# Optimization experiments

Measured on AMD Instinct MI355X. Metric: run time of the kernel, lower is better.

The kernel has to match this reference:

```python
import jax, jax.numpy as jnp
import numpy as np

B, T, D, DFF = 8, 2048, 1024, 4096
EPS = 1e-6
PLIF_ALPHA = 2.0


@jax.custom_vjp
def spike_fn(m):
    # hard threshold forward, atan surrogate backward (PLIF neuron)
    return (m > 0.0).astype(m.dtype)

def _spk_fwd(m):
    return (m > 0.0).astype(m.dtype), m

def _spk_bwd(m, g):
    ds = PLIF_ALPHA / (2.0 * (1.0 + (jnp.pi * 0.5 * PLIF_ALPHA * m) ** 2))
    return (g * ds,)

spike_fn.defvjp(_spk_fwd, _spk_bwd)


def _rmsnorm(x, w):
    rstd = jax.lax.rsqrt(jnp.mean(x * x, axis=-1, keepdims=True) + EPS)
    return x * rstd * w


def setup_inputs() -> dict:
    key = jax.random.key(0)
    ks = jax.random.split(key, 9)
    sc = 0.02
    return {
        'x': jax.random.normal(ks[0], (B, T, D), jnp.float32),
        'rms_w1': jnp.ones((D,), jnp.float32),
        'rms_w2': jnp.ones((D,), jnp.float32),
        'delta_w': sc * jax.random.normal(ks[1], (D, D), jnp.float32),
        'delta_b': jnp.zeros((D,), jnp.float32),
        'b_w': sc * jax.random.normal(ks[2], (D, D), jnp.float32),
        'b_b': jnp.zeros((D,), jnp.float32),
        'A_log': jnp.log(jnp.linspace(0.5, 2.0, D).astype(jnp.float32)),
        'log_tau': jnp.full((D,), jnp.log(2.0), jnp.float32),
        'plif_thr': jnp.ones((D,), jnp.float32),
        'syn_w': sc * jax.random.normal(ks[3], (D, D), jnp.float32),
        'syn_b': jnp.zeros((D,), jnp.float32),
        'gate_w': sc * jax.random.normal(ks[4], (D, D), jnp.float32),
        'gate_b': jnp.zeros((D,), jnp.float32),
        'ffn_g_w': sc * jax.random.normal(ks[5], (DFF, D), jnp.float32),
        'ffn_u_w': sc * jax.random.normal(ks[6], (DFF, D), jnp.float32),
        'ffn_d_w': sc * jax.random.normal(ks[7], (D, DFF), jnp.float32),
    }


def _forward(x, rms_w1, rms_w2, delta_w, delta_b, b_w, b_b, A_log, log_tau,
             plif_thr, syn_w, syn_b, gate_w, gate_b, ffn_g_w, ffn_u_w, ffn_d_w):
    Bx, Tx, Dx = x.shape
    # --- RMSNorm 1 ---
    y1 = _rmsnorm(x, rms_w1)
    # --- selective-scan style liquid inputs ---
    delta = jax.nn.softplus(jnp.einsum('btd,ed->bte', y1, delta_w) + delta_b)  # [B,T,D]
    bvec = delta * (jnp.einsum('btd,ed->bte', y1, b_w) + b_b)                  # [B,T,D]
    A = jnp.exp(-delta * jnp.exp(A_log))                                        # [B,T,D]

    # --- liquid recurrent scan: h_t = tanh(A_t * h_{t-1} + b_t) ---
    def liquid_step(h, ab):
        a_t, b_t = ab
        h = jnp.tanh(a_t * h + b_t)
        return h, h

    h0 = jnp.zeros((Bx, Dx), x.dtype)
    _, h_post = jax.lax.scan(liquid_step, h0,
                             (jnp.swapaxes(A, 0, 1), jnp.swapaxes(bvec, 0, 1)))
    h_post = jnp.swapaxes(h_post, 0, 1)  # [B,T,D]

    # --- PLIF spiking scan with soft reset ---
    pdec = jnp.exp(-1.0 / jnp.exp(log_tau))  # [D]

    def plif_step(v, h_t):
        v_pre = pdec * v + (1.0 - pdec) * h_t
        s = spike_fn(v_pre - plif_thr)
        return v_pre - s * plif_thr, s

    v0 = jnp.zeros((Bx, Dx), x.dtype)
    _, spike = jax.lax.scan(plif_step, v0, jnp.swapaxes(h_post, 0, 1))
    spike = jnp.swapaxes(spike, 0, 1)

    # --- SEW shortcut + synaptic gate ---
    spike_in = spike + h_post
    syn = jnp.einsum('btd,ed->bte', spike_in, syn_w) + syn_b
    gate = jax.nn.sigmoid(jnp.einsum('btd,ed->bte', spike_in, gate_w) + gate_b)
    x1 = x + syn * gate

    # --- RMSNorm 2 + SwiGLU FFN + residual ---
    y2 = _rmsnorm(x1, rms_w2)
    ffn_act = jax.nn.silu(y2 @ ffn_g_w.T) * (y2 @ ffn_u_w.T)
    return x1 + ffn_act @ ffn_d_w.T


def reference(x, rms_w1, rms_w2, delta_w, delta_b, b_w, b_b, A_log, log_tau,
              plif_thr, syn_w, syn_b, gate_w, gate_b, ffn_g_w, ffn_u_w, ffn_d_w):
    return _forward(x, rms_w1, rms_w2, delta_w, delta_b, b_w, b_b, A_log,
                    log_tau, plif_thr, syn_w, syn_b, gate_w, gate_b,
                    ffn_g_w, ffn_u_w, ffn_d_w)
```

## Files before the change

kernel.cpp:

```cpp
#include <hip/hip_runtime.h>
#include <stdint.h>

#define B_   8
#define T_   2048
#define D_   1024
#define DFF_ 4096
#define M_   (B_ * T_)

typedef __bf16 bf16;
typedef bf16  bf16x8 __attribute__((ext_vector_type(8)));
typedef bf16  bf16x4 __attribute__((ext_vector_type(4)));
typedef float f32x4  __attribute__((ext_vector_type(4)));

#define CAST_LDS(p) ((__attribute__((address_space(3))) void*)(p))
#define CAST_GLB(p) ((const __attribute__((address_space(1))) void*)(p))

struct CatArgs {
    const float* w1[3];
    const float* w2[3];
    bf16* dst[3];
    int end[3];
};

__global__ __launch_bounds__(256) void cvt_cat16_kernel(CatArgs a) {
    const int b = blockIdx.x;
    const int seg = (b >= a.end[0] ? 1 : 0) + (b >= a.end[1] ? 1 : 0);
    const int d = b - (seg ? a.end[seg - 1] : 0);
    const int rr = d & 31;
    const float* src = ((rr < 16) ? a.w1[seg] : a.w2[seg]) +
                       (size_t)(((d >> 5) << 4) + (d & 15)) * D_;
    bf16* dst = a.dst[seg] + (size_t)d * D_;
    const int t = threadIdx.x;
    const float4 v = ((const float4*)src)[t];
    bf16x4 o;
    o[0] = (bf16)v.x; o[1] = (bf16)v.y; o[2] = (bf16)v.z; o[3] = (bf16)v.w;
    ((bf16x4*)dst)[t] = o;
}

__global__ __launch_bounds__(256) void cvt_plain_kernel(const float* __restrict__ s,
                                                        bf16* __restrict__ d) {
    const int i = (blockIdx.x * 256 + threadIdx.x) * 4;
    const float4 v = *(const float4*)(s + i);
    bf16x4 o;
    o[0] = (bf16)v.x; o[1] = (bf16)v.y; o[2] = (bf16)v.z; o[3] = (bf16)v.w;
    *(bf16x4*)(d + i) = o;
}

__global__ __launch_bounds__(256) void rmsnorm_kernel(const float* __restrict__ x,
                                                      const float* __restrict__ w,
                                                      bf16* __restrict__ y) {
    const size_t row = blockIdx.x;
    const int t = threadIdx.x;
    const float4 v = ((const float4*)(x + row * D_))[t];
    float ss = v.x * v.x + v.y * v.y + v.z * v.z + v.w * v.w;
#pragma unroll
    for (int off = 32; off; off >>= 1) ss += __shfl_down(ss, off);
    __shared__ float red[4];
    if ((t & 63) == 0) red[t >> 6] = ss;
    __syncthreads();
    const float total = red[0] + red[1] + red[2] + red[3];
    const float rstd = rsqrtf(total * (1.0f / (float)D_) + 1e-6f);
    const float4 wv = ((const float4*)w)[t];
    bf16x4 o;
    o[0] = (bf16)(v.x * rstd * wv.x);
    o[1] = (bf16)(v.y * rstd * wv.y);
    o[2] = (bf16)(v.z * rstd * wv.z);
    o[3] = (bf16)(v.w * rstd * wv.w);
    ((bf16x4*)(y + row * D_))[t] = o;
}

__global__ __launch_bounds__(256) void rmsnorm_bf_kernel(const bf16* __restrict__ x,
                                                         const float* __restrict__ w,
                                                         bf16* __restrict__ y) {
    const size_t row = blockIdx.x;
    const int t = threadIdx.x;
    const bf16x4 xv = ((const bf16x4*)(x + row * D_))[t];
    float f0 = (float)xv[0], f1 = (float)xv[1], f2 = (float)xv[2], f3 = (float)xv[3];
    float ss = f0 * f0 + f1 * f1 + f2 * f2 + f3 * f3;
#pragma unroll
    for (int off = 32; off; off >>= 1) ss += __shfl_down(ss, off);
    __shared__ float red[4];
    if ((t & 63) == 0) red[t >> 6] = ss;
    __syncthreads();
    const float total = red[0] + red[1] + red[2] + red[3];
    const float rstd = rsqrtf(total * (1.0f / (float)D_) + 1e-6f);
    const float4 wv = ((const float4*)w)[t];
    bf16x4 o;
    o[0] = (bf16)(f0 * rstd * wv.x);
    o[1] = (bf16)(f1 * rstd * wv.y);
    o[2] = (bf16)(f2 * rstd * wv.z);
    o[3] = (bf16)(f3 * rstd * wv.w);
    ((bf16x4*)(y + row * D_))[t] = o;
}

#define SCAN_C  32
#define SCAN_L  (T_ / SCAN_C)
#define SCAN_W  32
#define SCAN_PF 8

template <int N, int W0>
__device__ __forceinline__ void scan_body(const uint32_t* __restrict__ p,
                                          bf16* __restrict__ o, const int ts,
                                          const float pdec, const float om,
                                          const float th) {
    uint32_t buf[SCAN_PF];
#pragma unroll
    for (int i = 0; i < SCAN_PF; ++i) buf[i] = p[(size_t)i * D_];
    float h = 0.0f, v = 0.0f;
#pragma unroll 8
    for (int k = 0; k < N; ++k) {
        const uint32_t w = buf[k & (SCAN_PF - 1)];
        if (k + SCAN_PF < N) buf[k & (SCAN_PF - 1)] = p[(size_t)(k + SCAN_PF) * D_];
        const float a  = __builtin_bit_cast(float, w << 16);
        const float bb = __builtin_bit_cast(float, w & 0xffff0000u);
        const float xv = fmaf(a, h, bb);
        const float e2 = __expf(2.0f * xv);
        h = 1.0f - __fdividef(2.0f, 1.0f + e2);
        const float vpre = fmaf(pdec, v, om * h);
        const float s = (vpre > th) ? 1.0f : 0.0f;
        v = vpre - s * th;
        if (k >= W0) o[(size_t)(ts + k) * D_] = (bf16)(s + h);
    }
}

__global__ __launch_bounds__(256) void scan_kernel(const uint32_t* __restrict__ ABp,
                                                   const float* __restrict__ log_tau,
                                                   const float* __restrict__ thr,
                                                   bf16* __restrict__ sp) {
    const int g = blockIdx.x * 256 + threadIdx.x;
    const int d = g & (D_ - 1);
    const int bc = g >> 10;
    const int b = bc / SCAN_C;
    const int c = bc % SCAN_C;
    const float pdec = __expf(-__expf(-log_tau[d]));
    const float om = 1.0f - pdec;
    const float th = thr[d];
    const int t0 = c * SCAN_L;
    const uint32_t* base = ABp + (size_t)b * (T_ * D_) + d;
    bf16* o = sp + (size_t)b * (T_ * D_) + d;
    if (c == 0) {
        scan_body<SCAN_L, 0>(base, o, 0, pdec, om, th);
    } else {
        const int ts = t0 - SCAN_W;
        scan_body<SCAN_L + SCAN_W, SCAN_W>(base + (size_t)ts * D_, o, ts, pdec, om, th);
    }
}


#define STG_A(kt, par, kh)                                                             \
  { bf16* l_ = lA0 + (((par) << 1) + (kh)) * 8192;                                     \
    const bf16* g_ = gA + (kt) * 64 + ((kh) << 5);                                     \
    __builtin_amdgcn_global_load_lds(CAST_GLB(g_), CAST_LDS(l_), 16, 0, 0);            \
    __builtin_amdgcn_global_load_lds(CAST_GLB(g_ + g2), CAST_LDS(l_ + 4096), 16, 0, 0); }
#define STG_B(gb, kt, par, kh)                                                         \
  { bf16* l_ = lB0 + (((par) << 1) + (kh)) * 8192;                                     \
    const bf16* g_ = (gb) + (kt) * 64 + ((kh) << 5);                                   \
    __builtin_amdgcn_global_load_lds(CAST_GLB(g_), CAST_LDS(l_), 16, 0, 0);            \
    __builtin_amdgcn_global_load_lds(CAST_GLB(g_ + g2), CAST_LDS(l_ + 4096), 16, 0, 0); }
#define DSREAD_A(KS, MH)                                                               \
  { const bf16* As_ = smA + (cb + (KS)) * 8192 + swz;                                  \
    _Pragma("unroll")                                                                  \
    for (int i = 0; i < 4; ++i)                                                        \
      af[i] = *(const bf16x8*)(As_ + (mr128 + (MH) * 64 + i * 16 + lane15) * 32);      \
  }
#define DSREAD_B(KS)                                                                   \
  { const bf16* Bs_ = smB + (cb + (KS)) * 8192 + swz;                                  \
    _Pragma("unroll")                                                                  \
    for (int j = 0; j < 4; ++j)                                                        \
      bfr[j] = *(const bf16x8*)(Bs_ + (nc64 + j * 16 + lane15) * 32);                  \
  }
#define MFMA16(MH)                                                                     \
  __builtin_amdgcn_s_setprio(1);                                                       \
  _Pragma("unroll")                                                                    \
  for (int i = 0; i < 4; ++i)                                                          \
    _Pragma("unroll")                                                                  \
    for (int j = 0; j < 4; ++j)                                                        \
      acc[(MH) * 4 + i][j] = __builtin_amdgcn_mfma_f32_16x16x32_bf16(                  \
          af[i], bfr[j], acc[(MH) * 4 + i][j], 0, 0, 0);                               \
  __builtin_amdgcn_s_setprio(0);
#define GBAR() __builtin_amdgcn_s_barrier()
#define LGKM0() asm volatile("s_waitcnt lgkmcnt(0)" ::: "memory")

template <int MODE>
__global__ __launch_bounds__(512, 2) void gemm8p_kernel(
    const bf16* __restrict__ A, const bf16* __restrict__ Bw,
    const int K, const int Nlog, const int NTN,
    const float* __restrict__ b1, const float* __restrict__ b2,
    const float* __restrict__ extra, const bf16* __restrict__ extra_bf,
    void* __restrict__ outp) {
    __shared__ bf16 smem[65536] __attribute__((aligned(16)));
    bf16* const smA = smem;
    bf16* const smB = smem + 32768;

    const int tid = threadIdx.x;
    const int wave = tid >> 6;
    const int lane = tid & 63;
    const int lane15 = lane & 15;
    const int quad = lane >> 4;
    const int mr = wave >> 2;
    const int nc = wave & 3;
    const int mr128 = mr * 128;
    const int nc64 = nc * 64;
    const int swz = (quad ^ ((lane15 >> 1) & 3)) << 3;

    const int xcd = blockIdx.x & 7;
    const int cu  = blockIdx.x >> 3;
    const int mt  = xcd * 8 + (cu & 7);
    const int nt0 = cu >> 3;
    const int TPB = NTN >> 2;
    const int NT  = K >> 6;
    const int S   = TPB * NT;

    const int srow = tid >> 2;
    const int scol = (((tid & 3) ^ ((srow >> 1) & 3)) << 3);
    const bf16* const gA = A + (size_t)(mt * 256 + srow) * K + scol;
    const size_t g2 = (size_t)128 * K;
    const size_t dB = (size_t)1024 * K;
    const bf16* gBc = Bw + (size_t)(nt0 * 256 + srow) * K + scol;
    bf16* const lA0 = smA + (wave << 9);
    bf16* const lB0 = smB + (wave << 9);

    f32x4 acc[8][4] = {};
    bf16x8 af[4];
    bf16x8 bfr[4];

    STG_B(gBc, 0, 0, 0); STG_A(0, 0, 0); STG_B(gBc, 0, 0, 1); STG_A(0, 0, 1);
    asm volatile("s_waitcnt vmcnt(4)" ::: "memory");
    STG_B(gBc, 1, 1, 0); STG_A(1, 1, 0); STG_B(gBc, 1, 1, 1);
    asm volatile("s_waitcnt vmcnt(6)" ::: "memory");
    GBAR();

    for (int w = 0; w < TPB; ++w) {
        const bf16* const gBn = gBc + dB;
        for (int t = 0; t < NT; ++t) {
            const int s = w * NT + t;
            const int cb = (t & 1) << 1;
            const int tp1 = (t + 1 == NT) ? 0 : t + 1;
            const int tp2 = (t + 2 >= NT) ? t + 2 - NT : t + 2;
            const int par1 = (t + 1) & 1;
            const int par2 = t & 1;
            const bf16* const gB2 = (t + 2 >= NT) ? gBn : gBc;
            const bool st1 = (s + 1 < S);
            const bool st2 = (s + 2 < S);

            DSREAD_A(0, 0); DSREAD_B(0);
            if (st1) STG_A(tp1, par1, 1);
            GBAR(); LGKM0();
            MFMA16(0);
            GBAR();

            DSREAD_A(0, 1);
            if (st2) STG_B(gB2, tp2, par2, 0);
            GBAR(); LGKM0();
            MFMA16(1);
            GBAR();

            DSREAD_A(1, 0); DSREAD_B(1);
            if (st2) STG_A(tp2, par2, 0);
            GBAR(); LGKM0();
            MFMA16(0);
            GBAR();

            DSREAD_A(1, 1);
            if (st2) {
                STG_B(gB2, tp2, par2, 1);
                asm volatile("s_waitcnt vmcnt(6)" ::: "memory");
            } else {
                asm volatile("s_waitcnt vmcnt(0)" ::: "memory");
            }
            GBAR(); LGKM0();
            MFMA16(1);
            GBAR();
        }

        if constexpr (MODE != 3) {
            const int nlog0 = (nt0 + w * 4) * 128 + nc * 32;
            const int mbase = mt * 256 + mr128;
#pragma unroll
            for (int i8 = 0; i8 < 8; ++i8)
#pragma unroll
                for (int jp = 0; jp < 2; ++jp)
#pragma unroll
                    for (int r = 0; r < 4; ++r) {
                        const int m = mbase + i8 * 16 + quad * 4 + r;
                        const int n = nlog0 + jp * 16 + lane15;
                        const size_t idx = (size_t)m * Nlog + n;
                        const float v1 = acc[i8][jp * 2][r];
                        const float v2 = acc[i8][jp * 2 + 1][r];
                        if constexpr (MODE == 0) {
                            const float dl = v1 + b1[n];
                            const float spv = (dl > 20.0f) ? dl : log1pf(__expf(dl));
                            const float bv = spv * (v2 + b2[n]);
                            const float av = __expf(-spv * __expf(extra[n]));
                            const uint32_t pa =
                                (uint32_t)__builtin_bit_cast(unsigned short, (bf16)av);
                            const uint32_t pb =
                                (uint32_t)__builtin_bit_cast(unsigned short, (bf16)bv);
                            ((uint32_t*)outp)[idx] = pa | (pb << 16);
                        } else if constexpr (MODE == 1) {
                            const float syn = v1 + b1[n];
                            const float z = v2 + b2[n];
                            const float gate = 1.0f / (1.0f + __expf(-z));
                            ((bf16*)outp)[idx] = (bf16)(extra[idx] + syn * gate);
                        } else {
                            const float sg = v1 / (1.0f + __expf(-v1));
                            ((bf16*)outp)[idx] = (bf16)(sg * v2);
                        }
                    }
        } else {
            const int mbase = mt * 256 + mr128;
            const int nbase = (nt0 + w * 4) * 256 + nc64;
#pragma unroll
            for (int i8 = 0; i8 < 8; ++i8)
#pragma unroll
                for (int j = 0; j < 4; ++j)
#pragma unroll
                    for (int r = 0; r < 4; ++r) {
                        const int m = mbase + i8 * 16 + quad * 4 + r;
                        const int n = nbase + j * 16 + lane15;
                        const size_t idx = (size_t)m * Nlog + n;
                        ((float*)outp)[idx] = (float)extra_bf[idx] + acc[i8][j][r];
                    }
        }

        if (w + 1 < TPB) {
#pragma unroll
            for (int i8 = 0; i8 < 8; ++i8)
#pragma unroll
                for (int j = 0; j < 4; ++j)
                    acc[i8][j] = (f32x4){0.0f, 0.0f, 0.0f, 0.0f};
            gBc = gBn;
        }
    }
}

#undef STG_A
#undef STG_B
#undef DSREAD_A
#undef DSREAD_B
#undef MFMA16
#undef GBAR
#undef LGKM0

extern "C" void kernel_launch(void* const* d_in, const int* in_sizes, int n_in,
                              void* d_out, int out_size, void* d_ws, size_t ws_size,
                              hipStream_t stream) {
    const float* x        = (const float*)d_in[0];
    const float* rms_w1   = (const float*)d_in[1];
    const float* rms_w2   = (const float*)d_in[2];
    const float* delta_w  = (const float*)d_in[3];
    const float* delta_b  = (const float*)d_in[4];
    const float* b_w      = (const float*)d_in[5];
    const float* b_b      = (const float*)d_in[6];
    const float* A_log    = (const float*)d_in[7];
    const float* log_tau  = (const float*)d_in[8];
    const float* plif_thr = (const float*)d_in[9];
    const float* syn_w    = (const float*)d_in[10];
    const float* syn_b    = (const float*)d_in[11];
    const float* gate_w   = (const float*)d_in[12];
    const float* gate_b   = (const float*)d_in[13];
    const float* ffn_g_w  = (const float*)d_in[14];
    const float* ffn_u_w  = (const float*)d_in[15];
    const float* ffn_d_w  = (const float*)d_in[16];

    char* ws = (char*)d_ws;
    const size_t MB = 1024ull * 1024ull;
    bf16* wcat_db = (bf16*)(ws + 0 * MB);
    bf16* wcat_sg = (bf16*)(ws + 4 * MB);
    bf16* wcat_gu = (bf16*)(ws + 8 * MB);
    bf16* wd      = (bf16*)(ws + 24 * MB);
    bf16*     y1      = (bf16*)(ws + 32 * MB);
    uint32_t* ABp     = (uint32_t*)(ws + 64 * MB);
    bf16*     spikein = (bf16*)(ws + 128 * MB);
    bf16* x1 = (bf16*)(ws + 160 * MB);
    bf16* y2 = (bf16*)(ws + 224 * MB);
    bf16* act = (bf16*)(ws + 32 * MB);
    float* outF = (float*)d_out;

    CatArgs ca;
    ca.w1[0] = delta_w; ca.w2[0] = b_w;     ca.dst[0] = wcat_db;
    ca.w1[1] = syn_w;   ca.w2[1] = gate_w;  ca.dst[1] = wcat_sg;
    ca.w1[2] = ffn_g_w; ca.w2[2] = ffn_u_w; ca.dst[2] = wcat_gu;
    ca.end[0] = 2048; ca.end[1] = 4096; ca.end[2] = 12288;
    cvt_cat16_kernel<<<12288, 256, 0, stream>>>(ca);
    cvt_plain_kernel<<<(D_ * DFF_) / 1024, 256, 0, stream>>>(ffn_d_w, wd);

    rmsnorm_kernel<<<M_, 256, 0, stream>>>(x, rms_w1, y1);

    gemm8p_kernel<0><<<256, 512, 0, stream>>>(
        y1, wcat_db, D_, D_, 8, delta_b, b_b, A_log, nullptr, ABp);

    scan_kernel<<<(B_ * SCAN_C * D_) / 256, 256, 0, stream>>>(ABp, log_tau, plif_thr, spikein);

    gemm8p_kernel<1><<<256, 512, 0, stream>>>(
        spikein, wcat_sg, D_, D_, 8, syn_b, gate_b, x, nullptr, x1);

    rmsnorm_bf_kernel<<<M_, 256, 0, stream>>>(x1, rms_w2, y2);

    gemm8p_kernel<2><<<256, 512, 0, stream>>>(
        y2, wcat_gu, D_, DFF_, 32, nullptr, nullptr, nullptr, nullptr, act);

    gemm8p_kernel<3><<<256, 512, 0, stream>>>(
        act, wd, DFF_, D_, 4, nullptr, nullptr, nullptr, x1, outF);
}
```

Before: 883.6 us.

## Merge prep kernels and double-buffer LDS fragment reads in GEMM pipeline

The two weight-conversion kernels and the first RMSNorm are merged into one launch that dispatches on block index, cutting launch gaps and tail effects. In the GEMM main loop, register fragments are double-buffered so the LDS reads for the next MFMA group are issued inside the high-priority region while the current MFMAs execute. This hides LDS latency behind matrix math at the cost of extra VGPRs, which could cause spills under the 512x2 launch bounds.

Measured after the change: 886.9 us, median of 4. No clear change (+0.4%).

```diff
diff --git a/kernel.cpp b/kernel.cpp
--- a/kernel.cpp
+++ b/kernel.cpp
@@ -15,58 +15,60 @@
 #define CAST_LDS(p) ((__attribute__((address_space(3))) void*)(p))
 #define CAST_GLB(p) ((const __attribute__((address_space(1))) void*)(p))
 
-struct CatArgs {
+struct PrepArgs {
     const float* w1[3];
     const float* w2[3];
     bf16* dst[3];
     int end[3];
+    const float* fd;
+    bf16* fdd;
+    const float* x;
+    const float* rw1;
+    bf16* y1;
 };
 
-__global__ __launch_bounds__(256) void cvt_cat16_kernel(CatArgs a) {
-    const int b = blockIdx.x;
-    const int seg = (b >= a.end[0] ? 1 : 0) + (b >= a.end[1] ? 1 : 0);
-    const int d = b - (seg ? a.end[seg - 1] : 0);
+__global__ __launch_bounds__(256) void prep_kernel(PrepArgs a) {
+    __shared__ float red[4];
+    const int blk = blockIdx.x;
+    const int t = threadIdx.x;
+
+    if (blk >= 16384) {
+        const size_t row = blk - 16384;
+        const float4 v = ((const float4*)(a.x + row * D_))[t];
+        float ss = v.x * v.x + v.y * v.y + v.z * v.z + v.w * v.w;
+#pragma unroll
+        for (int off = 32; off; off >>= 1) ss += __shfl_down(ss, off);
+        if ((t & 63) == 0) red[t >> 6] = ss;
+        __syncthreads();
+        const float total = red[0] + red[1] + red[2] + red[3];
+        const float rstd = rsqrtf(total * (1.0f / (float)D_) + 1e-6f);
+        const float4 wv = ((const float4*)a.rw1)[t];
+        bf16x4 o;
+        o[0] = (bf16)(v.x * rstd * wv.x);
+        o[1] = (bf16)(v.y * rstd * wv.y);
+        o[2] = (bf16)(v.z * rstd * wv.z);
+        o[3] = (bf16)(v.w * rstd * wv.w);
+        ((bf16x4*)(a.y1 + row * D_))[t] = o;
+        return;
+    }
+    if (blk >= 12288) {
+        const int i = ((blk - 12288) * 256 + t) * 4;
+        const float4 v = *(const float4*)(a.fd + i);
+        bf16x4 o;
+        o[0] = (bf16)v.x; o[1] = (bf16)v.y; o[2] = (bf16)v.z; o[3] = (bf16)v.w;
+        *(bf16x4*)(a.fdd + i) = o;
+        return;
+    }
+    const int seg = (blk >= a.end[0] ? 1 : 0) + (blk >= a.end[1] ? 1 : 0);
+    const int d = blk - (seg ? a.end[seg - 1] : 0);
     const int rr = d & 31;
     const float* src = ((rr < 16) ? a.w1[seg] : a.w2[seg]) +
                        (size_t)(((d >> 5) << 4) + (d & 15)) * D_;
     bf16* dst = a.dst[seg] + (size_t)d * D_;
-    const int t = threadIdx.x;
     const float4 v = ((const float4*)src)[t];
     bf16x4 o;
     o[0] = (bf16)v.x; o[1] = (bf16)v.y; o[2] = (bf16)v.z; o[3] = (bf16)v.w;
     ((bf16x4*)dst)[t] = o;
-}
-
-__global__ __launch_bounds__(256) void cvt_plain_kernel(const float* __restrict__ s,
-                                                        bf16* __restrict__ d) {
-    const int i = (blockIdx.x * 256 + threadIdx.x) * 4;
-    const float4 v = *(const float4*)(s + i);
-    bf16x4 o;
-    o[0] = (bf16)v.x; o[1] = (bf16)v.y; o[2] = (bf16)v.z; o[3] = (bf16)v.w;
-    *(bf16x4*)(d + i) = o;
-}
-
-__global__ __launch_bounds__(256) void rmsnorm_kernel(const float* __restrict__ x,
-                                                      const float* __restrict__ w,
-                                                      bf16* __restrict__ y) {
-    const size_t row = blockIdx.x;
-    const int t = threadIdx.x;
-    const float4 v = ((const float4*)(x + row * D_))[t];
-    float ss = v.x * v.x + v.y * v.y + v.z * v.z + v.w * v.w;
-#pragma unroll
-    for (int off = 32; off; off >>= 1) ss += __shfl_down(ss, off);
-    __shared__ float red[4];
-    if ((t & 63) == 0) red[t >> 6] = ss;
-    __syncthreads();
-    const float total = red[0] + red[1] + red[2] + red[3];
-    const float rstd = rsqrtf(total * (1.0f / (float)D_) + 1e-6f);
-    const float4 wv = ((const float4*)w)[t];
-    bf16x4 o;
-    o[0] = (bf16)(v.x * rstd * wv.x);
-    o[1] = (bf16)(v.y * rstd * wv.y);
-    o[2] = (bf16)(v.z * rstd * wv.z);
-    o[3] = (bf16)(v.w * rstd * wv.w);
-    ((bf16x4*)(y + row * D_))[t] = o;
 }
 
 __global__ __launch_bounds__(256) void rmsnorm_bf_kernel(const bf16* __restrict__ x,
@@ -157,27 +159,25 @@
     const bf16* g_ = (gb) + (kt) * 64 + ((kh) << 5);                                   \
     __builtin_amdgcn_global_load_lds(CAST_GLB(g_), CAST_LDS(l_), 16, 0, 0);            \
     __builtin_amdgcn_global_load_lds(CAST_GLB(g_ + g2), CAST_LDS(l_ + 4096), 16, 0, 0); }
-#define DSREAD_A(KS, MH)                                                               \
-  { const bf16* As_ = smA + (cb + (KS)) * 8192 + swz;                                  \
+#define PREF_A(dst, slot, MH)                                                          \
+  { const bf16* As_ = smA + (slot) * 8192 + swz;                                       \
     _Pragma("unroll")                                                                  \
     for (int i = 0; i < 4; ++i)                                                        \
-      af[i] = *(const bf16x8*)(As_ + (mr128 + (MH) * 64 + i * 16 + lane15) * 32);      \
+      dst[i] = *(const bf16x8*)(As_ + (mr128 + (MH) * 64 + i * 16 + lane15) * 32);     \
   }
-#define DSREAD_B(KS)                                                                   \
-  { const bf16* Bs_ = smB + (cb + (KS)) * 8192 + swz;                                  \
+#define PREF_B(dst, slot)                                                              \
+  { const bf16* Bs_ = smB + (slot) * 8192 + swz;                                       \
     _Pragma("unroll")                                                                  \
     for (int j = 0; j < 4; ++j)                                                        \
-      bfr[j] = *(const bf16x8*)(Bs_ + (nc64 + j * 16 + lane15) * 32);                  \
+      dst[j] = *(const bf16x8*)(Bs_ + (nc64 + j * 16 + lane15) * 32);                  \
   }
-#define MFMA16(MH)                                                                     \
-  __builtin_amdgcn_s_setprio(1);                                                       \
+#define MFMA16(A_, B_, MH)                                                             \
   _Pragma("unroll")                                                                    \
   for (int i = 0; i < 4; ++i)                                                          \
     _Pragma("unroll")                                                                  \
     for (int j = 0; j < 4; ++j)                                                        \
       acc[(MH) * 4 + i][j] = __builtin_amdgcn_mfma_f32_16x16x32_bf16(                  \
-          af[i], bfr[j], acc[(MH) * 4 + i][j], 0, 0, 0);                               \
-  __builtin_amdgcn_s_setprio(0);
+          A_[i], B_[j], acc[(MH) * 4 + i][j], 0, 0, 0);
 #define GBAR() __builtin_amdgcn_s_barrier()
 #define LGKM0() asm volatile("s_waitcnt lgkmcnt(0)" ::: "memory")
 
@@ -221,20 +221,22 @@
     bf16* const lB0 = smB + (wave << 9);
 
     f32x4 acc[8][4] = {};
-    bf16x8 af[4];
-    bf16x8 bfr[4];
+    bf16x8 a0[4], a1[4], b0[4], b1_[4];
 
     STG_B(gBc, 0, 0, 0); STG_A(0, 0, 0); STG_B(gBc, 0, 0, 1); STG_A(0, 0, 1);
     asm volatile("s_waitcnt vmcnt(4)" ::: "memory");
     STG_B(gBc, 1, 1, 0); STG_A(1, 1, 0); STG_B(gBc, 1, 1, 1);
     asm volatile("s_waitcnt vmcnt(6)" ::: "memory");
     GBAR();
+    PREF_A(a0, 0, 0);
+    PREF_B(b0, 0);
 
     for (int w = 0; w < TPB; ++w) {
         const bf16* const gBn = gBc + dB;
         for (int t = 0; t < NT; ++t) {
             const int s = w * NT + t;
             const int cb = (t & 1) << 1;
+            const int nb = cb ^ 2;
             const int tp1 = (t + 1 == NT) ? 0 : t + 1;
             const int tp2 = (t + 2 >= NT) ? t + 2 - NT : t + 2;
             const int par1 = (t + 1) & 1;
@@ -243,25 +245,31 @@
             const bool st1 = (s + 1 < S);
             const bool st2 = (s + 2 < S);
 
-            DSREAD_A(0, 0); DSREAD_B(0);
             if (st1) STG_A(tp1, par1, 1);
             GBAR(); LGKM0();
-            MFMA16(0);
+            __builtin_amdgcn_s_setprio(1);
+            PREF_A(a1, cb + 0, 1);
+            MFMA16(a0, b0, 0);
+            __builtin_amdgcn_s_setprio(0);
             GBAR();
 
-            DSREAD_A(0, 1);
             if (st2) STG_B(gB2, tp2, par2, 0);
             GBAR(); LGKM0();
-            MFMA16(1);
+            __builtin_amdgcn_s_setprio(1);
+            PREF_A(a0, cb + 1, 0);
+            PREF_B(b1_, cb + 1);
+            MFMA16(a1, b0, 1);
+            __builtin_amdgcn_s_setprio(0);
             GBAR();
 
-            DSREAD_A(1, 0); DSREAD_B(1);
             if (st2) STG_A(tp2, par2, 0);
             GBAR(); LGKM0();
-            MFMA16(0);
+            __builtin_amdgcn_s_setprio(1);
+            PREF_A(a1, cb + 1, 1);
+            MFMA16(a0, b1_, 0);
+            __builtin_amdgcn_s_setprio(0);
             GBAR();
 
-            DSREAD_A(1, 1);
             if (st2) {
                 STG_B(gB2, tp2, par2, 1);
                 asm volatile("s_waitcnt vmcnt(6)" ::: "memory");
@@ -269,7 +277,11 @@
                 asm volatile("s_waitcnt vmcnt(0)" ::: "memory");
             }
             GBAR(); LGKM0();
-            MFMA16(1);
+            __builtin_amdgcn_s_setprio(1);
+            PREF_A(a0, nb + 0, 0);
+            PREF_B(b0, nb + 0);
+            MFMA16(a1, b1_, 1);
+            __builtin_amdgcn_s_setprio(0);
             GBAR();
         }
 
@@ -336,8 +348,8 @@
 
 #undef STG_A
 #undef STG_B
-#undef DSREAD_A
-#undef DSREAD_B
+#undef PREF_A
+#undef PREF_B
 #undef MFMA16
 #undef GBAR
 #undef LGKM0
@@ -377,15 +389,14 @@
     bf16* act = (bf16*)(ws + 32 * MB);
     float* outF = (float*)d_out;
 
-    CatArgs ca;
-    ca.w1[0] = delta_w; ca.w2[0] = b_w;     ca.dst[0] = wcat_db;
-    ca.w1[1] = syn_w;   ca.w2[1] = gate_w;  ca.dst[1] = wcat_sg;
-    ca.w1[2] = ffn_g_w; ca.w2[2] = ffn_u_w; ca.dst[2] = wcat_gu;
-    ca.end[0] = 2048; ca.end[1] = 4096; ca.end[2] = 12288;
-    cvt_cat16_kernel<<<12288, 256, 0, stream>>>(ca);
-    cvt_plain_kernel<<<(D_ * DFF_) / 1024, 256, 0, stream>>>(ffn_d_w, wd);
-
-    rmsnorm_kernel<<<M_, 256, 0, stream>>>(x, rms_w1, y1);
+    PrepArgs pa;
+    pa.w1[0] = delta_w; pa.w2[0] = b_w;     pa.dst[0] = wcat_db;
+    pa.w1[1] = syn_w;   pa.w2[1] = gate_w;  pa.dst[1] = wcat_sg;
+    pa.w1[2] = ffn_g_w; pa.w2[2] = ffn_u_w; pa.dst[2] = wcat_gu;
+    pa.end[0] = 2048; pa.end[1] = 4096; pa.end[2] = 12288;
+    pa.fd = ffn_d_w; pa.fdd = wd;
+    pa.x = x; pa.rw1 = rms_w1; pa.y1 = y1;
+    prep_kernel<<<32768, 256, 0, stream>>>(pa);
 
     gemm8p_kernel<0><<<256, 512, 0, stream>>>(
         y1, wcat_db, D_, D_, 8, delta_b, b_b, A_log, nullptr, ABp);
```
